# Performance work log

Hardware: AMD Instinct MI355X
Metric: run time of the kernel (lower is better)

The kernel has to match this reference:

```python
import jax, jax.numpy as jnp
import numpy as np

N = 50000   # nodes per protein
F = 128     # v_feats
C = 128     # filters
K = 10      # neighbours


def setup_inputs() -> dict:
    key = jax.random.key(0)
    ks = jax.random.split(key, 9)
    return {
        "Z1": jax.random.normal(ks[0], (N, F), dtype=jnp.float32),
        "same1": jax.random.randint(ks[1], (N, K), -1, N),
        "diff1": jax.random.randint(ks[2], (N, K), -1, N),
        "Z2": jax.random.normal(ks[3], (N, F), dtype=jnp.float32),
        "same2": jax.random.randint(ks[4], (N, K), -1, N),
        "diff2": jax.random.randint(ks[5], (N, K), -1, N),
        "Wsv": jax.random.normal(ks[6], (F, C), dtype=jnp.float32),
        "Wsr": jax.random.normal(ks[7], (F, C), dtype=jnp.float32),
        "Wdr": jax.random.normal(ks[8], (F, C), dtype=jnp.float32),
    }


def _forward_protein(Z, same_neigh, diff_neigh, Wsv, Wsr, Wdr):
    node_signals = Z @ Wsv                    # [N, C]
    neigh_same = Z @ Wsr                      # [N, C]
    neigh_diff = Z @ Wdr                      # [N, C]
    mask_s = same_neigh > -1                  # [N, K]
    mask_d = diff_neigh > -1
    # gather neighbor signals, zero out padded (-1) slots
    same_feat = neigh_same[same_neigh] * mask_s[..., None].astype(Z.dtype)  # [N, K, C]
    diff_feat = neigh_diff[diff_neigh] * mask_d[..., None].astype(Z.dtype)
    # per-node valid-neighbor counts, clamped to 1 to avoid div-by-zero
    norm_s = jnp.maximum(mask_s.sum(axis=1), 1).astype(Z.dtype)[:, None]    # [N, 1]
    norm_d = jnp.maximum(mask_d.sum(axis=1), 1).astype(Z.dtype)[:, None]
    agg_s = same_feat.sum(axis=1) / norm_s    # mean over valid same-type neighbours
    agg_d = diff_feat.sum(axis=1) / norm_d
    return jax.nn.relu(node_signals + agg_s + agg_d)


def reference(Z1, same1, diff1, Z2, same2, diff2, Wsv, Wsr, Wdr):
    out1 = _forward_protein(Z1, same1, diff1, Wsv, Wsr, Wdr)
    out2 = _forward_protein(Z2, same2, diff2, Wsv, Wsr, Wdr)
    return (out1, out2)
```

## Files before the change

### kernel.cpp

```cpp
#include <hip/hip_runtime.h>
#include <cstdint>
#include <cstddef>

#define NN 50000
#define FF 128
#define CC 128
#define KK 10

constexpr int TILES_P = NN / 16;
constexpr size_t NC = (size_t)NN * CC;

typedef __bf16 bf16x8 __attribute__((ext_vector_type(8)));
typedef float  f32x4  __attribute__((ext_vector_type(4)));
typedef float  f32x2  __attribute__((ext_vector_type(2)));
typedef unsigned u32x2 __attribute__((ext_vector_type(2)));

__device__ __forceinline__ unsigned f2bf_u(float f) {
  union { float f; unsigned u; } x; x.f = f;
  unsigned r = x.u + 0x7fffu + ((x.u >> 16) & 1u);
  return r >> 16;
}

__global__ __launch_bounds__(256, 2)
void gemm3_kernel(const float* __restrict__ Z1, const float* __restrict__ Z2,
                  const float* __restrict__ Wsv, const float* __restrict__ Wsr,
                  const float* __restrict__ Wdr,
                  unsigned short* __restrict__ tblS, unsigned char* __restrict__ tbl8)
{
  const int tid  = threadIdx.x;
  const int wave = tid >> 6;
  const int lane = tid & 63;
  const int l15  = lane & 15;
  const int lg   = lane >> 4;
  const int col0 = wave * 32;

  const float* Wm[3] = { Wsv, Wsr, Wdr };
  bf16x8 b[3][2][4];
#pragma unroll
  for (int m = 0; m < 3; ++m) {
    const float* __restrict__ W = Wm[m];
#pragma unroll
    for (int j = 0; j < 2; ++j) {
      const int col = col0 + j * 16 + l15;
#pragma unroll
      for (int s = 0; s < 4; ++s) {
        bf16x8 f;
#pragma unroll
        for (int e = 0; e < 8; ++e) {
          const int k = s * 32 + (e >> 2) * 16 + lg * 4 + (e & 3);
          f[e] = (__bf16)W[k * CC + col];
        }
        b[m][j][s] = f;
      }
    }
  }

  const int total = 2 * TILES_P;
  for (int t = blockIdx.x; t < total; t += gridDim.x) {
    const int p    = t / TILES_P;
    const int row0 = (t - p * TILES_P) * 16;
    const float* __restrict__ Z = (p == 0) ? Z1 : Z2;
    const float* zrow = Z + (size_t)(row0 + l15) * FF;

    bf16x8 a[4];
#pragma unroll
    for (int s = 0; s < 4; ++s) {
      const f32x4 ha = *(const f32x4*)(zrow + s * 32 + lg * 4);
      const f32x4 hb = *(const f32x4*)(zrow + s * 32 + 16 + lg * 4);
      bf16x8 f;
      f[0] = (__bf16)ha.x; f[1] = (__bf16)ha.y; f[2] = (__bf16)ha.z; f[3] = (__bf16)ha.w;
      f[4] = (__bf16)hb.x; f[5] = (__bf16)hb.y; f[6] = (__bf16)hb.z; f[7] = (__bf16)hb.w;
      a[s] = f;
    }

    f32x4 acc[3][2] = {};
#pragma unroll
    for (int s = 0; s < 4; ++s)
#pragma unroll
      for (int m = 0; m < 3; ++m)
#pragma unroll
        for (int j = 0; j < 2; ++j)
          acc[m][j] = __builtin_amdgcn_mfma_f32_16x16x32_bf16(b[m][j][s], a[s], acc[m][j], 0, 0, 0);

    const int node = row0 + l15;
    unsigned short* tS  = tblS + (size_t)p * NC;
    unsigned char*  tRs = tbl8 + (size_t)(2 * p + 0) * NC;
    unsigned char*  tRd = tbl8 + (size_t)(2 * p + 1) * NC;
#pragma unroll
    for (int j = 0; j < 2; ++j) {
      const int cb = col0 + j * 16 + lg * 4;
      const size_t o = (size_t)node * CC + cb;

      u32x2 sv;
      sv.x = f2bf_u(acc[0][j][0]) | (f2bf_u(acc[0][j][1]) << 16);
      sv.y = f2bf_u(acc[0][j][2]) | (f2bf_u(acc[0][j][3]) << 16);
      *(u32x2*)(tS + o) = sv;

      int pk = __builtin_amdgcn_cvt_pk_fp8_f32(acc[1][j][0], acc[1][j][1], 0, false);
      pk     = __builtin_amdgcn_cvt_pk_fp8_f32(acc[1][j][2], acc[1][j][3], pk, true);
      *(unsigned*)(tRs + o) = (unsigned)pk;

      pk = __builtin_amdgcn_cvt_pk_fp8_f32(acc[2][j][0], acc[2][j][1], 0, false);
      pk = __builtin_amdgcn_cvt_pk_fp8_f32(acc[2][j][2], acc[2][j][3], pk, true);
      *(unsigned*)(tRd + o) = (unsigned)pk;
    }
  }
}

__global__ __launch_bounds__(256)
void agg_kernel(const int* __restrict__ same1, const int* __restrict__ diff1,
                const int* __restrict__ same2, const int* __restrict__ diff2,
                const unsigned short* __restrict__ tblS,
                const unsigned char* __restrict__ tbl8,
                float* __restrict__ out)
{
  const int lane = threadIdx.x & 63;
  const int g    = __builtin_amdgcn_readfirstlane(blockIdx.x * 4 + (threadIdx.x >> 6));
  const int p    = (g >= NN) ? 1 : 0;
  const int node = g - p * NN;
  const int* __restrict__ same = p ? same2 : same1;
  const int* __restrict__ diff = p ? diff2 : diff1;
  const unsigned char* __restrict__ tRs = tbl8 + (size_t)(2 * p + 0) * NC;
  const unsigned char* __restrict__ tRd = tbl8 + (size_t)(2 * p + 1) * NC;

  int idx[2 * KK];
#pragma unroll
  for (int k = 0; k < KK; ++k) {
    idx[k]      = same[node * KK + k];
    idx[KK + k] = diff[node * KK + k];
  }

  unsigned val[2 * KK];
#pragma unroll
  for (int i = 0; i < 2 * KK; ++i) {
    const unsigned char* __restrict__ t = (i < KK) ? tRs : tRd;
    const int ic = idx[i] < 0 ? 0 : idx[i];
    val[i] = *(const unsigned short*)(t + (size_t)ic * CC + lane * 2);
  }
  const size_t o = (size_t)g * CC + (size_t)(lane * 2);
  const unsigned su = *(const unsigned*)(tblS + o);

  asm volatile("" ::: "memory");

  float s0 = 0.f, s1 = 0.f, d0 = 0.f, d1 = 0.f;
  int sc = 0, dc = 0;
#pragma unroll
  for (int i = 0; i < KK; ++i) {
    sc += (idx[i] >= 0);
    const unsigned u = (idx[i] >= 0) ? val[i] : 0u;
    f32x2 pr = __builtin_amdgcn_cvt_pk_f32_fp8(u, false);
    s0 += pr.x; s1 += pr.y;
  }
#pragma unroll
  for (int i = KK; i < 2 * KK; ++i) {
    dc += (idx[i] >= 0);
    const unsigned u = (idx[i] >= 0) ? val[i] : 0u;
    f32x2 pr = __builtin_amdgcn_cvt_pk_f32_fp8(u, false);
    d0 += pr.x; d1 += pr.y;
  }

  union { unsigned u; float f; } slo, shi;
  slo.u = su << 16;
  shi.u = su & 0xFFFF0000u;

  const float fs = 1.f / (float)(sc > 0 ? sc : 1);
  const float fd = 1.f / (float)(dc > 0 ? dc : 1);
  const float vlo = slo.f + s0 * fs + d0 * fd;
  const float vhi = shi.f + s1 * fs + d1 * fd;
  f32x2 r;
  r.x = vlo > 0.f ? vlo : 0.f;
  r.y = vhi > 0.f ? vhi : 0.f;
  __builtin_nontemporal_store(r, (f32x2*)(out + o));
}

__global__ __launch_bounds__(128)
void fallback_kernel(const float* __restrict__ Z, const int* __restrict__ same,
                     const int* __restrict__ diff,
                     const float* __restrict__ Wsv, const float* __restrict__ Wsr,
                     const float* __restrict__ Wdr, float* __restrict__ out)
{
  const int node = blockIdx.x;
  const int c    = threadIdx.x;
  __shared__ float zs[FF];
  zs[c] = Z[(size_t)node * FF + c];
  __syncthreads();
  float sig = 0.f;
  for (int f = 0; f < FF; ++f) sig += zs[f] * Wsv[f * CC + c];

  float ssum = 0.f, dsum = 0.f;
  int scnt = 0, dcnt = 0;
  for (int k = 0; k < KK; ++k) {
    const int is = same[node * KK + k];
    if (is >= 0) {
      __syncthreads();
      zs[c] = Z[(size_t)is * FF + c];
      __syncthreads();
      float a = 0.f;
      for (int f = 0; f < FF; ++f) a += zs[f] * Wsr[f * CC + c];
      ssum += a; scnt++;
    }
  }
  for (int k = 0; k < KK; ++k) {
    const int id = diff[node * KK + k];
    if (id >= 0) {
      __syncthreads();
      zs[c] = Z[(size_t)id * FF + c];
      __syncthreads();
      float a = 0.f;
      for (int f = 0; f < FF; ++f) a += zs[f] * Wdr[f * CC + c];
      dsum += a; dcnt++;
    }
  }
  const float v = sig + ssum / (float)(scnt > 0 ? scnt : 1)
                      + dsum / (float)(dcnt > 0 ? dcnt : 1);
  out[(size_t)node * CC + c] = v > 0.f ? v : 0.f;
}

extern "C" void kernel_launch(void* const* d_in, const int* in_sizes, int n_in,
                              void* d_out, int out_size, void* d_ws, size_t ws_size,
                              hipStream_t stream)
{
  const float* Z1    = (const float*)d_in[0];
  const int*   same1 = (const int*)  d_in[1];
  const int*   diff1 = (const int*)  d_in[2];
  const float* Z2    = (const float*)d_in[3];
  const int*   same2 = (const int*)  d_in[4];
  const int*   diff2 = (const int*)  d_in[5];
  const float* Wsv   = (const float*)d_in[6];
  const float* Wsr   = (const float*)d_in[7];
  const float* Wdr   = (const float*)d_in[8];
  float* out = (float*)d_out;

  const size_t need = 8 * NC;
  unsigned short* tblS = (unsigned short*)d_ws;
  unsigned char*  tbl8 = (unsigned char*)d_ws + 2 * NC * sizeof(unsigned short);

  if (ws_size >= need) {
    gemm3_kernel<<<512, 256, 0, stream>>>(Z1, Z2, Wsv, Wsr, Wdr, tblS, tbl8);
    agg_kernel<<<(2 * NN) / 4, 256, 0, stream>>>(same1, diff1, same2, diff2,
                                                 tblS, tbl8, out);
  } else {
    fallback_kernel<<<NN, 128, 0, stream>>>(Z1, same1, diff1, Wsv, Wsr, Wdr, out);
    fallback_kernel<<<NN, 128, 0, stream>>>(Z2, same2, diff2, Wsv, Wsr, Wdr, out + NC);
  }
}
```

Measured before the change: 93.28 us.

## Prefetch next Z tile in registers and split columns over eight waves

```diff
diff --git a/kernel.cpp b/kernel.cpp
--- a/kernel.cpp
+++ b/kernel.cpp
@@ -21,7 +21,7 @@
   return r >> 16;
 }
 
-__global__ __launch_bounds__(256, 2)
+__global__ __launch_bounds__(512, 4)
 void gemm3_kernel(const float* __restrict__ Z1, const float* __restrict__ Z2,
                   const float* __restrict__ Wsv, const float* __restrict__ Wsr,
                   const float* __restrict__ Wdr,
@@ -32,78 +32,101 @@
   const int lane = tid & 63;
   const int l15  = lane & 15;
   const int lg   = lane >> 4;
-  const int col0 = wave * 32;
+  const int wcol = wave * 16;
 
   const float* Wm[3] = { Wsv, Wsr, Wdr };
-  bf16x8 b[3][2][4];
+  bf16x8 b[3][4];
 #pragma unroll
   for (int m = 0; m < 3; ++m) {
     const float* __restrict__ W = Wm[m];
-#pragma unroll
-    for (int j = 0; j < 2; ++j) {
-      const int col = col0 + j * 16 + l15;
-#pragma unroll
-      for (int s = 0; s < 4; ++s) {
-        bf16x8 f;
-#pragma unroll
-        for (int e = 0; e < 8; ++e) {
-          const int k = s * 32 + (e >> 2) * 16 + lg * 4 + (e & 3);
-          f[e] = (__bf16)W[k * CC + col];
-        }
-        b[m][j][s] = f;
+    const int col = wcol + l15;
+#pragma unroll
+    for (int s = 0; s < 4; ++s) {
+      bf16x8 f;
+#pragma unroll
+      for (int e = 0; e < 8; ++e) {
+        const int k = s * 32 + (e >> 2) * 16 + lg * 4 + (e & 3);
+        f[e] = (__bf16)W[k * CC + col];
       }
+      b[m][s] = f;
     }
   }
 
   const int total = 2 * TILES_P;
-  for (int t = blockIdx.x; t < total; t += gridDim.x) {
+  int t = blockIdx.x;
+  if (t >= total) return;
+
+  f32x4 pre[8];
+  {
     const int p    = t / TILES_P;
     const int row0 = (t - p * TILES_P) * 16;
     const float* __restrict__ Z = (p == 0) ? Z1 : Z2;
     const float* zrow = Z + (size_t)(row0 + l15) * FF;
-
+#pragma unroll
+    for (int s = 0; s < 4; ++s) {
+      pre[s]     = *(const f32x4*)(zrow + s * 32 + lg * 4);
+      pre[4 + s] = *(const f32x4*)(zrow + s * 32 + 16 + lg * 4);
+    }
+  }
+
+  while (true) {
     bf16x8 a[4];
 #pragma unroll
     for (int s = 0; s < 4; ++s) {
-      const f32x4 ha = *(const f32x4*)(zrow + s * 32 + lg * 4);
-      const f32x4 hb = *(const f32x4*)(zrow + s * 32 + 16 + lg * 4);
+      const f32x4 ha = pre[s];
+      const f32x4 hb = pre[4 + s];
       bf16x8 f;
       f[0] = (__bf16)ha.x; f[1] = (__bf16)ha.y; f[2] = (__bf16)ha.z; f[3] = (__bf16)ha.w;
       f[4] = (__bf16)hb.x; f[5] = (__bf16)hb.y; f[6] = (__bf16)hb.z; f[7] = (__bf16)hb.w;
       a[s] = f;
     }
 
-    f32x4 acc[3][2] = {};
+    const int tc = t;
+    t += gridDim.x;
+    if (t < total) {
+      const int p    = t / TILES_P;
+      const int row0 = (t - p * TILES_P) * 16;
+      const float* __restrict__ Z = (p == 0) ? Z1 : Z2;
+      const float* zrow = Z + (size_t)(row0 + l15) * FF;
+#pragma unroll
+      for (int s = 0; s < 4; ++s) {
+        pre[s]     = *(const f32x4*)(zrow + s * 32 + lg * 4);
+        pre[4 + s] = *(const f32x4*)(zrow + s * 32 + 16 + lg * 4);
+      }
+    }
+
+    f32x4 acc[3] = {};
 #pragma unroll
     for (int s = 0; s < 4; ++s)
 #pragma unroll
       for (int m = 0; m < 3; ++m)
-#pragma unroll
-        for (int j = 0; j < 2; ++j)
-          acc[m][j] = __builtin_amdgcn_mfma_f32_16x16x32_bf16(b[m][j][s], a[s], acc[m][j], 0, 0, 0);
-
-    const int node = row0 + l15;
-    unsigned short* tS  = tblS + (size_t)p * NC;
-    unsigned char*  tRs = tbl8 + (size_t)(2 * p + 0) * NC;
-    unsigned char*  tRd = tbl8 + (size_t)(2 * p + 1) * NC;
-#pragma unroll
-    for (int j = 0; j < 2; ++j) {
-      const int cb = col0 + j * 16 + lg * 4;
+        acc[m] = __builtin_amdgcn_mfma_f32_16x16x32_bf16(b[m][s], a[s], acc[m], 0, 0, 0);
+
+    {
+      const int p    = tc / TILES_P;
+      const int row0 = (tc - p * TILES_P) * 16;
+      const int node = row0 + l15;
+      const int cb   = wcol + lg * 4;
       const size_t o = (size_t)node * CC + cb;
+      unsigned short* tS  = tblS + (size_t)p * NC;
+      unsigned char*  tRs = tbl8 + (size_t)(2 * p + 0) * NC;
+      unsigned char*  tRd = tbl8 + (size_t)(2 * p + 1) * NC;
 
       u32x2 sv;
-      sv.x = f2bf_u(acc[0][j][0]) | (f2bf_u(acc[0][j][1]) << 16);
-      sv.y = f2bf_u(acc[0][j][2]) | (f2bf_u(acc[0][j][3]) << 16);
+      sv.x = f2bf_u(acc[0][0]) | (f2bf_u(acc[0][1]) << 16);
+      sv.y = f2bf_u(acc[0][2]) | (f2bf_u(acc[0][3]) << 16);
       *(u32x2*)(tS + o) = sv;
 
-      int pk = __builtin_amdgcn_cvt_pk_fp8_f32(acc[1][j][0], acc[1][j][1], 0, false);
-      pk     = __builtin_amdgcn_cvt_pk_fp8_f32(acc[1][j][2], acc[1][j][3], pk, true);
+      int pk = __builtin_amdgcn_cvt_pk_fp8_f32(acc[1][0], acc[1][1], 0, false);
+      pk     = __builtin_amdgcn_cvt_pk_fp8_f32(acc[1][2], acc[1][3], pk, true);
       *(unsigned*)(tRs + o) = (unsigned)pk;
 
-      pk = __builtin_amdgcn_cvt_pk_fp8_f32(acc[2][j][0], acc[2][j][1], 0, false);
-      pk = __builtin_amdgcn_cvt_pk_fp8_f32(acc[2][j][2], acc[2][j][3], pk, true);
+      pk = __builtin_amdgcn_cvt_pk_fp8_f32(acc[2][0], acc[2][1], 0, false);
+      pk = __builtin_amdgcn_cvt_pk_fp8_f32(acc[2][2], acc[2][3], pk, true);
       *(unsigned*)(tRd + o) = (unsigned)pk;
     }
+
+    if (t >= total) break;
   }
 }
 
@@ -236,7 +259,7 @@
   unsigned char*  tbl8 = (unsigned char*)d_ws + 2 * NC * sizeof(unsigned short);
 
   if (ws_size >= need) {
-    gemm3_kernel<<<512, 256, 0, stream>>>(Z1, Z2, Wsv, Wsr, Wdr, tblS, tbl8);
+    gemm3_kernel<<<512, 512, 0, stream>>>(Z1, Z2, Wsv, Wsr, Wdr, tblS, tbl8);
     agg_kernel<<<(2 * NN) / 4, 256, 0, stream>>>(same1, diff1, same2, diff2,
                                                  tblS, tbl8, out);
   } else {
```

Result: slower. 107.8 us (+15.5%).
